# Optimization experiments

Measured on AMD Instinct MI355X. Metric: run time of the kernel, lower is better.

The kernel has to match this reference:

```python
import jax, jax.numpy as jnp
import numpy as np

B, T, C, H = 8, 2048, 1024, 128  # batch, seq (== block_size), embed dim, head size


def setup_inputs() -> dict:
    key = jax.random.key(0)
    kx, kq, kk, kv = jax.random.split(key, 4)
    x = jax.random.normal(kx, (B, T, C), dtype=jnp.float32)
    # torch Linear(no bias) weights: [head_size, in_features], applied as x @ W.T
    s = 1.0 / np.sqrt(C)
    Wq = jax.random.normal(kq, (H, C), dtype=jnp.float32) * s
    Wk = jax.random.normal(kk, (H, C), dtype=jnp.float32) * s
    Wv = jax.random.normal(kv, (H, C), dtype=jnp.float32) * s
    return {"x": x, "Wq": Wq, "Wk": Wk, "Wv": Wv}


def reference(x, Wq, Wk, Wv):
    # projections: [B,T,C] @ [C,H] -> [B,T,H]
    q = jnp.einsum('btc,hc->bth', x, Wq)
    k = jnp.einsum('btc,hc->bth', x, Wk)
    v = jnp.einsum('btc,hc->bth', x, Wv)
    scale = k.shape[-1] ** -0.5
    # scores [B,T,T], causal mask, softmax in fp32 (autocast disabled in original)
    scores = jnp.einsum('bqh,bkh->bqk', q, k) * scale
    causal = jnp.tril(jnp.ones((T, T), dtype=bool))
    scores = jnp.where(causal, scores, -jnp.inf)
    attn = jax.nn.softmax(scores.astype(jnp.float32), axis=-1)
    # dropout_rate = 0.0 -> identity
    out = jnp.einsum('bqk,bkh->bqh', attn.astype(v.dtype), v)
    return out
```

## Files before the change

kernel.cpp:

```cpp
#include <hip/hip_runtime.h>
#include <hip/hip_bf16.h>

constexpr int NB = 8;
constexpr int T  = 2048;
constexpr int C  = 1024;
constexpr int Hd = 128;

typedef short bf16x8 __attribute__((ext_vector_type(8)));
typedef float floatx4 __attribute__((ext_vector_type(4)));

__device__ __forceinline__ ushort f2bf(float x) {
    return __builtin_bit_cast(ushort, __float2bfloat16(x));
}
__device__ __forceinline__ float bf2f(ushort u) {
    unsigned int x = ((unsigned int)u) << 16;
    return __builtin_bit_cast(float, x);
}
__device__ __forceinline__ void async16(ushort* lds, const ushort* g) {
    __builtin_amdgcn_global_load_lds(
        (const __attribute__((address_space(1))) unsigned int*)g,
        (__attribute__((address_space(3))) unsigned int*)lds, 16, 0, 0);
}

__global__ __launch_bounds__(256) void convert_xw(
    const float* __restrict__ X, const float* __restrict__ Wq,
    const float* __restrict__ Wk, const float* __restrict__ Wv,
    ushort* __restrict__ Xb, ushort* __restrict__ Wb)
{
    int bid = blockIdx.x;
    if (bid < 8192) {
        size_t i = ((size_t)bid * 256 + threadIdx.x) * 8;
        float4 a = *(const float4*)&X[i];
        float4 b = *(const float4*)&X[i + 4];
        bf16x8 o;
        o[0] = (short)f2bf(a.x); o[1] = (short)f2bf(a.y);
        o[2] = (short)f2bf(a.z); o[3] = (short)f2bf(a.w);
        o[4] = (short)f2bf(b.x); o[5] = (short)f2bf(b.y);
        o[6] = (short)f2bf(b.z); o[7] = (short)f2bf(b.w);
        *(bf16x8*)&Xb[i] = o;
    } else {
        int g = (bid - 8192) * 256 + threadIdx.x;
        size_t base = (size_t)g * 8;
        int sel = (int)(base >> 17);
        const float* W = sel == 0 ? Wq : (sel == 1 ? Wk : Wv);
        float s = (sel == 0) ? 0.12751744f : 1.0f;
        size_t off = base - (size_t)sel * 131072;
        float4 a = *(const float4*)&W[off];
        float4 b = *(const float4*)&W[off + 4];
        bf16x8 o;
        o[0] = (short)f2bf(a.x * s); o[1] = (short)f2bf(a.y * s);
        o[2] = (short)f2bf(a.z * s); o[3] = (short)f2bf(a.w * s);
        o[4] = (short)f2bf(b.x * s); o[5] = (short)f2bf(b.y * s);
        o[6] = (short)f2bf(b.z * s); o[7] = (short)f2bf(b.w * s);
        *(bf16x8*)&Wb[base] = o;
    }
}

__global__ __launch_bounds__(256) void qkv_gemm(
    const ushort* __restrict__ Xb, const ushort* __restrict__ Wb,
    ushort* __restrict__ Qo, ushort* __restrict__ Ko, ushort* __restrict__ Vt)
{
    __shared__ ushort SM[32768];
    const int m0 = blockIdx.x * 128;
    const int n0 = blockIdx.y * 128;
    const int tid = threadIdx.x, lane = tid & 63, wave = tid >> 6;
    const int quad = lane >> 4, colL = lane & 15;
    const int wm = (wave & 1) * 64, wn = (wave >> 1) * 64;
    const int lr = lane >> 3;
    const int lcs = ((lane & 7) ^ (lr & 7)) * 8;

    floatx4 acc[4][4] = {};

    #define QKV_STAGE(buf, kt)                                                   \
        {                                                                        \
            const int k0_ = (kt) * 64;                                           \
            ushort* Ab_ = SM + (buf) * 16384;                                    \
            ushort* Bb_ = SM + (buf) * 16384 + 8192;                             \
            for (int t = 0; t < 4; ++t) {                                        \
                int q = wave * 4 + t;                                            \
                async16(&Ab_[q * 512 + lane * 8],                                \
                        &Xb[(size_t)(m0 + q * 8 + lr) * C + k0_ + lcs]);         \
            }                                                                    \
            for (int t = 0; t < 4; ++t) {                                        \
                int q = wave * 4 + t;                                            \
                async16(&Bb_[q * 512 + lane * 8],                                \
                        &Wb[(size_t)(n0 + q * 8 + lr) * C + k0_ + lcs]);         \
            }                                                                    \
        }

    QKV_STAGE(0, 0)

    for (int kt = 0; kt < 16; ++kt) {
        const int cur = kt & 1;
        __syncthreads();

        if (kt + 1 < 16) QKV_STAGE(cur ^ 1, kt + 1)

        const ushort* Ab = SM + cur * 16384;
        const ushort* Bb = SM + cur * 16384 + 8192;
        for (int kk = 0; kk < 2; ++kk) {
            bf16x8 af[4], bfr[4];
            const int g = ((kk * 4 + quad) ^ (colL & 7)) * 8;
            for (int mt = 0; mt < 4; ++mt)
                af[mt] = *(const bf16x8*)&Ab[(wm + mt * 16 + colL) * 64 + g];
            for (int nt = 0; nt < 4; ++nt)
                bfr[nt] = *(const bf16x8*)&Bb[(wn + nt * 16 + colL) * 64 + g];
            for (int mt = 0; mt < 4; ++mt)
                for (int nt = 0; nt < 4; ++nt)
                    acc[mt][nt] = __builtin_amdgcn_mfma_f32_16x16x32_bf16(
                        af[mt], bfr[nt], acc[mt][nt], 0, 0, 0);
        }
    }
    #undef QKV_STAGE

    const int sel = n0 >> 7;
    if (sel < 2) {
        ushort* dst = sel == 0 ? Qo : Ko;
        for (int mt = 0; mt < 4; ++mt)
            for (int nt = 0; nt < 4; ++nt)
                for (int r = 0; r < 4; ++r) {
                    int row = m0 + wm + mt * 16 + quad * 4 + r;
                    int h = wn + nt * 16 + colL;
                    dst[(size_t)row * Hd + h] = f2bf(acc[mt][nt][r]);
                }
    } else {
        __syncthreads();
        ushort* TL = SM;
        for (int mt = 0; mt < 4; ++mt)
            for (int nt = 0; nt < 4; ++nt)
                for (int r = 0; r < 4; ++r)
                    TL[(wm + mt * 16 + quad * 4 + r) * 130 + wn + nt * 16 + colL] =
                        f2bf(acc[mt][nt][r]);
        __syncthreads();
        const int b = m0 >> 11, tb = m0 & 2047;
        const int h = tid & 127, tq = tid >> 7;
        for (int st = 0; st < 8; ++st) {
            int t0 = tq * 64 + st * 8;
            bf16x8 o;
            for (int jx = 0; jx < 8; ++jx)
                o[jx] = (short)TL[(t0 + jx) * 130 + h];
            *(bf16x8*)&Vt[((size_t)b * Hd + h) * T + tb + t0] = o;
        }
    }
}

__global__ __launch_bounds__(256, 2) void attn_partial(
    const ushort* __restrict__ Q, const ushort* __restrict__ Kg,
    const ushort* __restrict__ Vt, ushort* __restrict__ Opart,
    float* __restrict__ lpart)
{
    __shared__ ushort Kl[128 * 128];
    __shared__ ushort Vl[128 * 128];

    const int tid = threadIdx.x, lane = tid & 63, wave = tid >> 6;
    const int quad = lane >> 4, colL = lane & 15;

    const int id = blockIdx.x;
    const int s  = id & 3;
    const int bq = id >> 2;
    const int b  = bq & 7;
    const int qt = 31 - (bq >> 3);
    const int q0 = qt * 64;
    const int cmax = (q0 + 63) >> 7;

    const int r16 = tid >> 4, p16 = tid & 15;

    bf16x8 qa[4];
    {
        const ushort* qp =
            &Q[((size_t)b * T + q0 + wave * 16 + colL) * Hd + quad * 8];
        for (int ks = 0; ks < 4; ++ks)
            qa[ks] = *(const bf16x8*)&qp[ks * 32];
    }

    floatx4 Oacc[8] = {};
    float l_p[4] = {0.f, 0.f, 0.f, 0.f};

    if (s <= cmax) {
        {
            const int k0 = s * 128;
            for (int t = 0; t < 8; ++t) {
                int row = t * 16 + r16;
                async16(&Kl[t * 2048 + tid * 8],
                        &Kg[((size_t)b * T + k0 + row) * Hd + ((p16 ^ (row & 15)) * 8)]);
            }
            for (int t = 0; t < 8; ++t) {
                int hrow = t * 16 + r16;
                async16(&Vl[t * 2048 + tid * 8],
                        &Vt[((size_t)b * Hd + hrow) * T + k0 + ((p16 ^ (hrow & 15)) * 8)]);
            }
        }

        for (int c = s; c <= cmax; c += 4) {
            __syncthreads();

            floatx4 accS[8] = {};
            for (int ks = 0; ks < 4; ++ks)
                for (int nt = 0; nt < 8; ++nt) {
                    int krow = nt * 16 + colL;
                    bf16x8 kb = *(const bf16x8*)
                        &Kl[krow * 128 + (((ks * 4 + quad) ^ colL) * 8)];
                    accS[nt] = __builtin_amdgcn_mfma_f32_16x16x32_bf16(qa[ks], kb, accS[nt], 0, 0, 0);
                }

            if (c == cmax) {
                const int k0 = c * 128;
                for (int nt = 0; nt < 8; ++nt)
                    for (int rr = 0; rr < 4; ++rr) {
                        int lrow = q0 + wave * 16 + quad * 4 + rr;
                        int lcol = k0 + nt * 16 + colL;
                        if (lcol > lrow) accS[nt][rr] = -__builtin_inff();
                    }
            }
            __syncthreads();

            ushort* Pw = &Kl[wave * 2048];
            for (int nt = 0; nt < 8; ++nt)
                for (int rr = 0; rr < 4; ++rr) {
                    float p = __builtin_amdgcn_exp2f(fminf(accS[nt][rr], 14.f));
                    l_p[rr] += p;
                    int prow = quad * 4 + rr;
                    Pw[prow * 128 + ((nt * 16 + colL) ^ ((prow & 7) << 4))] = f2bf(p);
                }

            bf16x8 pa[4];
            {
                const int prow = colL;
                const int sw = (prow & 7) << 4;
                for (int ks = 0; ks < 4; ++ks)
                    pa[ks] = *(const bf16x8*)&Pw[prow * 128 + ((ks * 32 + quad * 8) ^ sw)];
            }
            __syncthreads();

            if (c + 4 <= cmax) {
                const int k0 = (c + 4) * 128;
                for (int t = 0; t < 8; ++t) {
                    int row = t * 16 + r16;
                    async16(&Kl[t * 2048 + tid * 8],
                            &Kg[((size_t)b * T + k0 + row) * Hd + ((p16 ^ (row & 15)) * 8)]);
                }
            }

            for (int ks = 0; ks < 4; ++ks)
                for (int th = 0; th < 8; ++th) {
                    int hrow = th * 16 + colL;
                    bf16x8 vb = *(const bf16x8*)
                        &Vl[hrow * 128 + (((ks * 4 + quad) ^ colL) * 8)];
                    Oacc[th] = __builtin_amdgcn_mfma_f32_16x16x32_bf16(pa[ks], vb, Oacc[th], 0, 0, 0);
                }

            if (c + 4 <= cmax) {
                __syncthreads();
                const int k0 = (c + 4) * 128;
                for (int t = 0; t < 8; ++t) {
                    int hrow = t * 16 + r16;
                    async16(&Vl[t * 2048 + tid * 8],
                            &Vt[((size_t)b * Hd + hrow) * T + k0 + ((p16 ^ (hrow & 15)) * 8)]);
                }
            }
        }
    }

    float l_r[4];
    for (int rr = 0; rr < 4; ++rr) {
        float v = l_p[rr];
        for (int off = 1; off < 16; off <<= 1)
            v += __shfl_xor(v, off, 64);
        l_r[rr] = v;
    }
    ushort* Op = &Opart[(size_t)id * 8192];
    for (int th = 0; th < 8; ++th)
        for (int rr = 0; rr < 4; ++rr) {
            int row = wave * 16 + quad * 4 + rr;
            Op[row * 128 + th * 16 + colL] = f2bf(Oacc[th][rr]);
        }
    if (colL == 0)
        for (int rr = 0; rr < 4; ++rr) {
            int row = wave * 16 + quad * 4 + rr;
            lpart[(size_t)id * 64 + row] = l_r[rr];
        }
}

__global__ __launch_bounds__(256) void attn_combine(
    const ushort* __restrict__ Opart, const float* __restrict__ lpart,
    float* __restrict__ out)
{
    const int bq = blockIdx.x;
    const int b  = bq & 7;
    const int qt = 31 - (bq >> 3);
    const int t = threadIdx.x;
    const int row_l = t >> 2;
    const int c32 = (t & 3) * 32;

    float l = 0.f;
    for (int s = 0; s < 4; ++s)
        l += lpart[(size_t)(bq * 4 + s) * 64 + row_l];
    const float inv = 1.0f / l;

    float acc[32];
#pragma unroll
    for (int i = 0; i < 32; ++i) acc[i] = 0.f;
    for (int s = 0; s < 4; ++s) {
        const ushort* p = &Opart[(size_t)(bq * 4 + s) * 8192 + row_l * 128 + c32];
#pragma unroll
        for (int x = 0; x < 4; ++x) {
            bf16x8 a = *(const bf16x8*)&p[x * 8];
#pragma unroll
            for (int i2 = 0; i2 < 8; ++i2)
                acc[x * 8 + i2] += bf2f((ushort)a[i2]);
        }
    }
    float* dst = &out[((size_t)b * T + qt * 64 + row_l) * Hd + c32];
#pragma unroll
    for (int x = 0; x < 8; ++x) {
        float4 o;
        o.x = acc[x * 4 + 0] * inv;
        o.y = acc[x * 4 + 1] * inv;
        o.z = acc[x * 4 + 2] * inv;
        o.w = acc[x * 4 + 3] * inv;
        *(float4*)&dst[x * 4] = o;
    }
}

extern "C" void kernel_launch(void* const* d_in, const int* in_sizes, int n_in,
                              void* d_out, int out_size, void* d_ws, size_t ws_size,
                              hipStream_t stream) {
    const float* x  = (const float*)d_in[0];
    const float* Wq = (const float*)d_in[1];
    const float* Wk = (const float*)d_in[2];
    const float* Wv = (const float*)d_in[3];
    float* out = (float*)d_out;

    char* w = (char*)d_ws;
    ushort* Xb = (ushort*)w;
    ushort* Opart = (ushort*)w;
    float* lpart  = (float*)(w + (size_t)1024 * 8192 * 2);
    w += (size_t)33554432;
    ushort* Wb = (ushort*)w;  w += (size_t)786432;
    ushort* Qb  = (ushort*)w;  w += (size_t)NB * T * Hd * 2;
    ushort* Kb  = (ushort*)w;  w += (size_t)NB * T * Hd * 2;
    ushort* Vtb = (ushort*)w;  w += (size_t)NB * T * Hd * 2;

    convert_xw<<<8384, 256, 0, stream>>>(x, Wq, Wk, Wv, Xb, Wb);
    qkv_gemm<<<dim3(128, 3), 256, 0, stream>>>(Xb, Wb, Qb, Kb, Vtb);
    attn_partial<<<1024, 256, 0, stream>>>(Qb, Kb, Vtb, Opart, lpart);
    attn_combine<<<256, 256, 0, stream>>>(Opart, lpart, out);
}
```

Before: 150.9 us.

## Fuse fp32-to-bf16 conversion into QKV GEMM and combine into attention

Drops the separate conversion kernel: the QKV GEMM now loads fp32 X and W straight from global memory into registers, converts them to bf16 (applying the Q scale) and writes them to swizzled LDS, with register double-buffering in place of async global-to-LDS copies. The combine kernel is folded into attn_partial through a per-query-tile atomic counter, so the last-finishing split block does the reduction. This saves two launches and the bf16 X round trip through HBM. In exchange the GEMM reads twice the bytes of fp32 input, loses the async LDS loads, and each split block pays an atomic plus threadfence.

Measured after the change: 383.0 us. 154% more time.

```diff
diff --git a/kernel.cpp b/kernel.cpp
--- a/kernel.cpp
+++ b/kernel.cpp
@@ -22,79 +22,70 @@
         (__attribute__((address_space(3))) unsigned int*)lds, 16, 0, 0);
 }
 
-__global__ __launch_bounds__(256) void convert_xw(
+__global__ __launch_bounds__(256) void qkv_fused(
     const float* __restrict__ X, const float* __restrict__ Wq,
     const float* __restrict__ Wk, const float* __restrict__ Wv,
-    ushort* __restrict__ Xb, ushort* __restrict__ Wb)
-{
-    int bid = blockIdx.x;
-    if (bid < 8192) {
-        size_t i = ((size_t)bid * 256 + threadIdx.x) * 8;
-        float4 a = *(const float4*)&X[i];
-        float4 b = *(const float4*)&X[i + 4];
-        bf16x8 o;
-        o[0] = (short)f2bf(a.x); o[1] = (short)f2bf(a.y);
-        o[2] = (short)f2bf(a.z); o[3] = (short)f2bf(a.w);
-        o[4] = (short)f2bf(b.x); o[5] = (short)f2bf(b.y);
-        o[6] = (short)f2bf(b.z); o[7] = (short)f2bf(b.w);
-        *(bf16x8*)&Xb[i] = o;
-    } else {
-        int g = (bid - 8192) * 256 + threadIdx.x;
-        size_t base = (size_t)g * 8;
-        int sel = (int)(base >> 17);
-        const float* W = sel == 0 ? Wq : (sel == 1 ? Wk : Wv);
-        float s = (sel == 0) ? 0.12751744f : 1.0f;
-        size_t off = base - (size_t)sel * 131072;
-        float4 a = *(const float4*)&W[off];
-        float4 b = *(const float4*)&W[off + 4];
-        bf16x8 o;
-        o[0] = (short)f2bf(a.x * s); o[1] = (short)f2bf(a.y * s);
-        o[2] = (short)f2bf(a.z * s); o[3] = (short)f2bf(a.w * s);
-        o[4] = (short)f2bf(b.x * s); o[5] = (short)f2bf(b.y * s);
-        o[6] = (short)f2bf(b.z * s); o[7] = (short)f2bf(b.w * s);
-        *(bf16x8*)&Wb[base] = o;
-    }
-}
-
-__global__ __launch_bounds__(256) void qkv_gemm(
-    const ushort* __restrict__ Xb, const ushort* __restrict__ Wb,
-    ushort* __restrict__ Qo, ushort* __restrict__ Ko, ushort* __restrict__ Vt)
+    ushort* __restrict__ Qo, ushort* __restrict__ Ko, ushort* __restrict__ Vt,
+    int* __restrict__ cnt)
 {
     __shared__ ushort SM[32768];
     const int m0 = blockIdx.x * 128;
-    const int n0 = blockIdx.y * 128;
+    const int sel = blockIdx.y;
+    const float* Wp = sel == 0 ? Wq : (sel == 1 ? Wk : Wv);
+    const float wscale = sel == 0 ? 0.12751744f : 1.0f;
     const int tid = threadIdx.x, lane = tid & 63, wave = tid >> 6;
     const int quad = lane >> 4, colL = lane & 15;
     const int wm = (wave & 1) * 64, wn = (wave >> 1) * 64;
-    const int lr = lane >> 3;
-    const int lcs = ((lane & 7) ^ (lr & 7)) * 8;
+    const int r8 = tid >> 3, g8 = tid & 7;
+    const int swz = (g8 ^ (r8 & 7)) * 8;
+
+    if (blockIdx.x == 0 && sel == 0) cnt[tid] = 0;
 
     floatx4 acc[4][4] = {};
-
-    #define QKV_STAGE(buf, kt)                                                   \
-        {                                                                        \
-            const int k0_ = (kt) * 64;                                           \
-            ushort* Ab_ = SM + (buf) * 16384;                                    \
-            ushort* Bb_ = SM + (buf) * 16384 + 8192;                             \
-            for (int t = 0; t < 4; ++t) {                                        \
-                int q = wave * 4 + t;                                            \
-                async16(&Ab_[q * 512 + lane * 8],                                \
-                        &Xb[(size_t)(m0 + q * 8 + lr) * C + k0_ + lcs]);         \
-            }                                                                    \
-            for (int t = 0; t < 4; ++t) {                                        \
-                int q = wave * 4 + t;                                            \
-                async16(&Bb_[q * 512 + lane * 8],                                \
-                        &Wb[(size_t)(n0 + q * 8 + lr) * C + k0_ + lcs]);         \
-            }                                                                    \
-        }
-
-    QKV_STAGE(0, 0)
+    floatx4 ax[4][2], bx[4][2];
+
+    #define QKV_LOAD(kt)                                                        \
+        {                                                                       \
+            const int k0_ = (kt) * 64;                                          \
+            _Pragma("unroll")                                                   \
+            for (int t = 0; t < 4; ++t) {                                       \
+                const float* xp = &X[(size_t)(m0 + t * 32 + r8) * C + k0_ + g8 * 8]; \
+                const float* wp = &Wp[(size_t)(t * 32 + r8) * C + k0_ + g8 * 8];\
+                ax[t][0] = *(const floatx4*)xp;                                 \
+                ax[t][1] = *(const floatx4*)(xp + 4);                           \
+                bx[t][0] = *(const floatx4*)wp;                                 \
+                bx[t][1] = *(const floatx4*)(wp + 4);                           \
+            }                                                                   \
+        }
+
+    #define QKV_WRITE(buf)                                                      \
+        {                                                                       \
+            ushort* Ab_ = SM + (buf) * 16384;                                   \
+            ushort* Bb_ = Ab_ + 8192;                                           \
+            _Pragma("unroll")                                                   \
+            for (int t = 0; t < 4; ++t) {                                       \
+                const int off = (t * 32 + r8) * 64 + swz;                       \
+                bf16x8 oa, ob;                                                  \
+                _Pragma("unroll")                                               \
+                for (int j = 0; j < 4; ++j) {                                   \
+                    oa[j]     = (short)f2bf(ax[t][0][j]);                       \
+                    oa[4 + j] = (short)f2bf(ax[t][1][j]);                       \
+                    ob[j]     = (short)f2bf(bx[t][0][j] * wscale);              \
+                    ob[4 + j] = (short)f2bf(bx[t][1][j] * wscale);              \
+                }                                                               \
+                *(bf16x8*)&Ab_[off] = oa;                                       \
+                *(bf16x8*)&Bb_[off] = ob;                                       \
+            }                                                                   \
+        }
+
+    QKV_LOAD(0)
+    QKV_WRITE(0)
 
     for (int kt = 0; kt < 16; ++kt) {
         const int cur = kt & 1;
         __syncthreads();
 
-        if (kt + 1 < 16) QKV_STAGE(cur ^ 1, kt + 1)
+        if (kt + 1 < 16) QKV_LOAD(kt + 1)
 
         const ushort* Ab = SM + cur * 16384;
         const ushort* Bb = SM + cur * 16384 + 8192;
@@ -110,10 +101,12 @@
                     acc[mt][nt] = __builtin_amdgcn_mfma_f32_16x16x32_bf16(
                         af[mt], bfr[nt], acc[mt][nt], 0, 0, 0);
         }
-    }
-    #undef QKV_STAGE
-
-    const int sel = n0 >> 7;
+
+        if (kt + 1 < 16) QKV_WRITE(cur ^ 1)
+    }
+    #undef QKV_LOAD
+    #undef QKV_WRITE
+
     if (sel < 2) {
         ushort* dst = sel == 0 ? Qo : Ko;
         for (int mt = 0; mt < 4; ++mt)
@@ -147,10 +140,11 @@
 __global__ __launch_bounds__(256, 2) void attn_partial(
     const ushort* __restrict__ Q, const ushort* __restrict__ Kg,
     const ushort* __restrict__ Vt, ushort* __restrict__ Opart,
-    float* __restrict__ lpart)
+    float* __restrict__ lpart, float* __restrict__ out, int* __restrict__ cnt)
 {
     __shared__ ushort Kl[128 * 128];
     __shared__ ushort Vl[128 * 128];
+    __shared__ int lastFlag;
 
     const int tid = threadIdx.x, lane = tid & 63, wave = tid >> 6;
     const int quad = lane >> 4, colL = lane & 15;
@@ -279,46 +273,44 @@
             int row = wave * 16 + quad * 4 + rr;
             lpart[(size_t)id * 64 + row] = l_r[rr];
         }
-}
-
-__global__ __launch_bounds__(256) void attn_combine(
-    const ushort* __restrict__ Opart, const float* __restrict__ lpart,
-    float* __restrict__ out)
-{
-    const int bq = blockIdx.x;
-    const int b  = bq & 7;
-    const int qt = 31 - (bq >> 3);
-    const int t = threadIdx.x;
-    const int row_l = t >> 2;
-    const int c32 = (t & 3) * 32;
-
-    float l = 0.f;
-    for (int s = 0; s < 4; ++s)
-        l += lpart[(size_t)(bq * 4 + s) * 64 + row_l];
-    const float inv = 1.0f / l;
-
-    float acc[32];
+
+    __threadfence();
+    if (tid == 0)
+        lastFlag = (atomicAdd(&cnt[bq], 1) == 3);
+    __syncthreads();
+    if (lastFlag) {
+        __threadfence();
+        const int row_l = tid >> 2;
+        const int c32 = (tid & 3) * 32;
+
+        float l = 0.f;
+        for (int s4 = 0; s4 < 4; ++s4)
+            l += lpart[(size_t)(bq * 4 + s4) * 64 + row_l];
+        const float inv = 1.0f / l;
+
+        float accO[32];
 #pragma unroll
-    for (int i = 0; i < 32; ++i) acc[i] = 0.f;
-    for (int s = 0; s < 4; ++s) {
-        const ushort* p = &Opart[(size_t)(bq * 4 + s) * 8192 + row_l * 128 + c32];
+        for (int i = 0; i < 32; ++i) accO[i] = 0.f;
+        for (int s4 = 0; s4 < 4; ++s4) {
+            const ushort* p = &Opart[(size_t)(bq * 4 + s4) * 8192 + row_l * 128 + c32];
 #pragma unroll
-        for (int x = 0; x < 4; ++x) {
-            bf16x8 a = *(const bf16x8*)&p[x * 8];
+            for (int x = 0; x < 4; ++x) {
+                bf16x8 a = *(const bf16x8*)&p[x * 8];
 #pragma unroll
-            for (int i2 = 0; i2 < 8; ++i2)
-                acc[x * 8 + i2] += bf2f((ushort)a[i2]);
-        }
-    }
-    float* dst = &out[((size_t)b * T + qt * 64 + row_l) * Hd + c32];
+                for (int i2 = 0; i2 < 8; ++i2)
+                    accO[x * 8 + i2] += bf2f((ushort)a[i2]);
+            }
+        }
+        float* dst = &out[((size_t)b * T + qt * 64 + row_l) * Hd + c32];
 #pragma unroll
-    for (int x = 0; x < 8; ++x) {
-        float4 o;
-        o.x = acc[x * 4 + 0] * inv;
-        o.y = acc[x * 4 + 1] * inv;
-        o.z = acc[x * 4 + 2] * inv;
-        o.w = acc[x * 4 + 3] * inv;
-        *(float4*)&dst[x * 4] = o;
+        for (int x = 0; x < 8; ++x) {
+            float4 o;
+            o.x = accO[x * 4 + 0] * inv;
+            o.y = accO[x * 4 + 1] * inv;
+            o.z = accO[x * 4 + 2] * inv;
+            o.w = accO[x * 4 + 3] * inv;
+            *(float4*)&dst[x * 4] = o;
+        }
     }
 }
 
@@ -332,17 +324,13 @@
     float* out = (float*)d_out;
 
     char* w = (char*)d_ws;
-    ushort* Xb = (ushort*)w;
-    ushort* Opart = (ushort*)w;
-    float* lpart  = (float*)(w + (size_t)1024 * 8192 * 2);
-    w += (size_t)33554432;
-    ushort* Wb = (ushort*)w;  w += (size_t)786432;
     ushort* Qb  = (ushort*)w;  w += (size_t)NB * T * Hd * 2;
     ushort* Kb  = (ushort*)w;  w += (size_t)NB * T * Hd * 2;
     ushort* Vtb = (ushort*)w;  w += (size_t)NB * T * Hd * 2;
-
-    convert_xw<<<8384, 256, 0, stream>>>(x, Wq, Wk, Wv, Xb, Wb);
-    qkv_gemm<<<dim3(128, 3), 256, 0, stream>>>(Xb, Wb, Qb, Kb, Vtb);
-    attn_partial<<<1024, 256, 0, stream>>>(Qb, Kb, Vtb, Opart, lpart);
-    attn_combine<<<256, 256, 0, stream>>>(Opart, lpart, out);
-}
+    ushort* Opart = (ushort*)w;  w += (size_t)1024 * 8192 * 2;
+    float* lpart = (float*)w;    w += (size_t)1024 * 64 * 4;
+    int* cnt = (int*)w;          w += 256 * 4;
+
+    qkv_fused<<<dim3(128, 3), 256, 0, stream>>>(x, Wq, Wk, Wv, Qb, Kb, Vtb, cnt);
+    attn_partial<<<1024, 256, 0, stream>>>(Qb, Kb, Vtb, Opart, lpart, out, cnt);
+}
```
